# Performance work log

Measured on AMD Instinct MI355X. Metric: run time of the kernel, lower is better.

The kernel has to match this reference:

```python
import jax, jax.numpy as jnp
import numpy as np

EPS = 1e-6
ALPHA = 0.1
BETA = 0.25


def setup_inputs() -> dict:
    key = jax.random.key(0)
    k1, k2, k3 = jax.random.split(key, 3)
    B, C, D = 4096, 256, 128
    x = jax.random.normal(k1, (B, D), dtype=jnp.float32)
    prev_q = jax.random.normal(k2, (B, D), dtype=jnp.float32)
    codes = jax.random.normal(k3, (1, C, D), dtype=jnp.float32)
    return {"x": x, "prev_q": prev_q, "codes": codes}


def compute_distance(x, codes):
    # x: (B, D); codes: (1, C, D) or (B, 1, D) -> (B, C) / (B, 1); metric='l2'
    return jnp.sum((x[:, None, :] - codes) ** 2, axis=-1)


def get_rotation_matrix(u, v, eps=EPS):
    # u: (B, D) normalized; v: (D,) normalized -> R: (B, D, D)
    B, D = u.shape
    uvT = u[:, :, None] * v[None, None, :]          # (B, D, D) = u v^T
    vuT = v[None, :, None] * u[:, None, :]          # (B, D, D) = v u^T
    A = uvT - vuT
    A2 = jnp.einsum('bik,bkj->bij', A, A)
    dot = jnp.einsum('bd,d->b', u, v)[:, None, None]
    I = jnp.eye(D, dtype=u.dtype)
    return I + A + A2 / (1.0 + dot + eps)


def reference(x, prev_q, codes):
    B, D = x.shape
    v = jnp.ones((D,), dtype=x.dtype) / jnp.sqrt(jnp.asarray(D, x.dtype))
    # F.normalize(prev_q, dim=-1, eps=1e-6)
    n = jnp.linalg.norm(prev_q, axis=-1, keepdims=True)
    u = prev_q / jnp.maximum(n, EPS)
    R = get_rotation_matrix(u, v)
    # x_canonical = R^T x
    x_canonical = jnp.einsum('bji,bj->bi', R, x)
    raw_distances = compute_distance(x_canonical, codes)        # (B, C)
    distances = raw_distances / D / ALPHA
    # eval path: argmin + gather
    indices = jnp.argmin(distances, axis=-1)                    # (B,)
    quantized_canonical = codes[0][indices]                     # (B, D)
    quantized = jnp.einsum('bij,bj->bi', R, quantized_canonical)
    loss_commit = compute_distance(x, jax.lax.stop_gradient(quantized)[:, None, :]).mean()
    loss_codebook = compute_distance(jax.lax.stop_gradient(x), quantized[:, None, :]).mean()
    loss = loss_commit + BETA * loss_codebook
    return quantized, indices, loss
```

## Files before the change

kernel.cpp:

```cpp
#include <hip/hip_runtime.h>

#define BD 4096
#define CD 256
#define DD 128
#define RB 16
#define TB 1024

__global__ __launch_bounds__(TB) void rq_fused(
    const float* __restrict__ x,
    const float* __restrict__ pq,
    const float* __restrict__ codes,
    float* __restrict__ out)
{
    __shared__ __align__(16) char pool[CD * DD * 4
                                       + RB * DD * 4
                                       + CD * 4
                                       + RB * 4 * 4
                                       + RB * 4
                                       + RB * 4];
    float*  code_s = (float*)pool;
    float4* mb4    = (float4*)pool;
    float*  xc_s   = (float*)(pool + CD * DD * 4);
    float*  cn2_s  = xc_s + RB * DD;
    float*  row_c  = cn2_s + CD;
    float*  row_s  = row_c + RB;
    float*  row_invn = row_s + RB;
    int*    row_idx  = (int*)(row_invn + 2 * RB);
    float*  loss_s   = (float*)(row_idx + RB);

    const int tid  = threadIdx.x;
    const int wv   = tid >> 6;
    const int lane = tid & 63;
    const int row0 = blockIdx.x * RB;
    const float INV_SQRT_D = 0.088388347648318447f;

    const size_t growA = (size_t)(row0 + wv);
    const float2 xv = ((const float2*)(x  + growA * DD))[lane];
    const float2 pv = ((const float2*)(pq + growA * DD))[lane];

    {
        #pragma unroll
        for (int k = 0; k < 8; ++k) {
            const int f = k * TB + tid;
            const int g = f ^ ((f >> 5) & 7);
            __builtin_amdgcn_global_load_lds(
                (const __attribute__((address_space(1))) uint32_t*)(codes + (size_t)g * 4),
                (__attribute__((address_space(3))) uint32_t*)(code_s + (size_t)f * 4),
                16, 0, 0);
        }
    }

    {
        const int r = wv;
        float s0 = pv.x * pv.x + pv.y * pv.y;
        float s1 = pv.x + pv.y;
        float s2 = xv.x + xv.y;
        float s3 = pv.x * xv.x + pv.y * xv.y;
        #pragma unroll
        for (int m = 32; m > 0; m >>= 1) {
            s0 += __shfl_xor(s0, m);
            s1 += __shfl_xor(s1, m);
            s2 += __shfl_xor(s2, m);
            s3 += __shfl_xor(s3, m);
        }
        const float invn = 1.0f / fmaxf(sqrtf(s0), 1e-6f);
        const float b = s2 * INV_SQRT_D;
        const float a = s3 * invn;
        const float c = s1 * invn * INV_SQRT_D;
        const float s = 1.0f / (1.0f + c + 1e-6f);
        const float au = -b + s * (c * b - a);
        const float av =  a + s * (c * a - b);
        float2 o;
        o.x = xv.x + au * (pv.x * invn) + av * INV_SQRT_D;
        o.y = xv.y + au * (pv.y * invn) + av * INV_SQRT_D;
        ((float2*)(xc_s + r * DD))[lane] = o;
        if (lane == 0) { row_c[r] = c; row_s[r] = s; row_invn[r] = invn; }
    }
    __syncthreads();

    {
        const int c = tid >> 2, q = tid & 3;
        const int sw = c & 7;
        const float* cp = code_s + c * DD + q * 32;
        float n2 = 0.f;
        #pragma unroll
        for (int i = 0; i < 8; ++i) {
            const float4 v = *(const float4*)(cp + ((i ^ sw) << 2));
            n2 = fmaf(v.x, v.x, n2); n2 = fmaf(v.y, v.y, n2);
            n2 = fmaf(v.z, v.z, n2); n2 = fmaf(v.w, v.w, n2);
        }
        n2 += __shfl_xor(n2, 1);
        n2 += __shfl_xor(n2, 2);
        if (q == 0) cn2_s[c] = n2;
    }
    __syncthreads();

    const int rg = wv & 3, dq = wv >> 2;
    float xreg[4];
    #pragma unroll
    for (int rr = 0; rr < 4; ++rr)
        xreg[rr] = xc_s[(rg * 4 + rr) * DD + dq * 32 + (lane & 31)];
    const int sw = lane & 7;
    const float* cb = code_s + lane * DD + dq * 32;
    float acc[4][4] = {};
    #define RL(rr, j) __int_as_float(__builtin_amdgcn_readlane(__float_as_int(xreg[rr]), (j)))
    #pragma unroll
    for (int i = 0; i < 8; ++i) {
        const int off = (i ^ sw) << 2;
        const float4 c0 = *(const float4*)(cb + off);
        const float4 c1 = *(const float4*)(cb +  64 * DD + off);
        const float4 c2 = *(const float4*)(cb + 128 * DD + off);
        const float4 c3 = *(const float4*)(cb + 192 * DD + off);
        #pragma unroll
        for (int r = 0; r < 4; ++r) {
            const float y0 = RL(r, 4 * i + 0), y1 = RL(r, 4 * i + 1);
            const float y2 = RL(r, 4 * i + 2), y3 = RL(r, 4 * i + 3);
            acc[0][r] = fmaf(c0.x, y0, acc[0][r]); acc[0][r] = fmaf(c0.y, y1, acc[0][r]);
            acc[0][r] = fmaf(c0.z, y2, acc[0][r]); acc[0][r] = fmaf(c0.w, y3, acc[0][r]);
            acc[1][r] = fmaf(c1.x, y0, acc[1][r]); acc[1][r] = fmaf(c1.y, y1, acc[1][r]);
            acc[1][r] = fmaf(c1.z, y2, acc[1][r]); acc[1][r] = fmaf(c1.w, y3, acc[1][r]);
            acc[2][r] = fmaf(c2.x, y0, acc[2][r]); acc[2][r] = fmaf(c2.y, y1, acc[2][r]);
            acc[2][r] = fmaf(c2.z, y2, acc[2][r]); acc[2][r] = fmaf(c2.w, y3, acc[2][r]);
            acc[3][r] = fmaf(c3.x, y0, acc[3][r]); acc[3][r] = fmaf(c3.y, y1, acc[3][r]);
            acc[3][r] = fmaf(c3.z, y2, acc[3][r]); acc[3][r] = fmaf(c3.w, y3, acc[3][r]);
        }
    }
    #undef RL

    __syncthreads();
    if (dq != 0) {
        const int e = (rg * 3 + (dq - 1)) * 64 + lane;
        #pragma unroll
        for (int t = 0; t < 4; ++t) {
            float4 w;
            w.x = acc[t][0]; w.y = acc[t][1]; w.z = acc[t][2]; w.w = acc[t][3];
            mb4[t * 768 + e] = w;
        }
    }
    __syncthreads();
    if (dq == 0) {
        #pragma unroll
        for (int s = 0; s < 3; ++s) {
            const int e = (rg * 3 + s) * 64 + lane;
            #pragma unroll
            for (int t = 0; t < 4; ++t) {
                const float4 pm = mb4[t * 768 + e];
                acc[t][0] += pm.x; acc[t][1] += pm.y; acc[t][2] += pm.z; acc[t][3] += pm.w;
            }
        }
        const float cn0  = cn2_s[lane];
        const float cn1  = cn2_s[lane + 64];
        const float cn2v = cn2_s[lane + 128];
        const float cn3  = cn2_s[lane + 192];
        float bv[4]; int bi[4];
        #pragma unroll
        for (int r = 0; r < 4; ++r) {
            float v0 = fmaf(-2.f, acc[0][r], cn0); int i0 = lane;
            const float v1 = fmaf(-2.f, acc[1][r], cn1);
            const float v2 = fmaf(-2.f, acc[2][r], cn2v);
            const float v3 = fmaf(-2.f, acc[3][r], cn3);
            if (v1 < v0) { v0 = v1; i0 = lane + 64;  }
            if (v2 < v0) { v0 = v2; i0 = lane + 128; }
            if (v3 < v0) { v0 = v3; i0 = lane + 192; }
            bv[r] = v0; bi[r] = i0;
        }
        #pragma unroll
        for (int m = 1; m < 64; m <<= 1) {
            #pragma unroll
            for (int r = 0; r < 4; ++r) {
                const float ov = __shfl_xor(bv[r], m);
                const int   oi = __shfl_xor(bi[r], m);
                if (ov < bv[r] || (ov == bv[r] && oi < bi[r])) { bv[r] = ov; bi[r] = oi; }
            }
        }
        if (lane == 0) {
            #pragma unroll
            for (int r = 0; r < 4; ++r) {
                row_idx[rg * 4 + r] = bi[r];
                out[(size_t)BD * DD + row0 + rg * 4 + r] = (float)bi[r];
            }
        }
    }
    __syncthreads();

    {
        const int r = wv;
        const int qi = row_idx[r];
        const float invn = row_invn[r];
        const float c = row_c[r];
        const float s = row_s[r];
        const float2 q = ((const float2*)(codes + (size_t)qi * DD))[lane];
        float pd = pv.x * q.x + pv.y * q.y;
        float ws = q.x + q.y;
        #pragma unroll
        for (int m = 32; m > 0; m >>= 1) {
            pd += __shfl_xor(pd, m);
            ws += __shfl_xor(ws, m);
        }
        const float pp = pd * invn;
        const float w  = ws * INV_SQRT_D;
        const float bu  =  w + s * (c * w - pp);
        const float bvv = -pp + s * (c * pp - w);
        float2 o;
        o.x = q.x + bu * (pv.x * invn) + bvv * INV_SQRT_D;
        o.y = q.y + bu * (pv.y * invn) + bvv * INV_SQRT_D;
        ((float2*)(out + growA * DD))[lane] = o;

        float dx = xv.x - o.x;
        float ls = dx * dx;
        dx = xv.y - o.y;
        ls = fmaf(dx, dx, ls);
        #pragma unroll
        for (int m = 32; m > 0; m >>= 1) ls += __shfl_xor(ls, m);
        if (lane == 0) loss_s[r] = ls;
    }
    __syncthreads();
    if (tid == 0) {
        float tot = 0.f;
        #pragma unroll
        for (int r = 0; r < RB; ++r) tot += loss_s[r];
        atomicAdd(out + (size_t)BD * DD + BD, tot * (1.25f / (float)BD));
    }
}

extern "C" void kernel_launch(void* const* d_in, const int* in_sizes, int n_in,
                              void* d_out, int out_size, void* d_ws, size_t ws_size,
                              hipStream_t stream) {
    const float* xin   = (const float*)d_in[0];
    const float* prevq = (const float*)d_in[1];
    const float* codes = (const float*)d_in[2];
    float* out = (float*)d_out;
    rq_fused<<<BD / RB, TB, 0, stream>>>(xin, prevq, codes, out);
}
```

Measured before the change: 74.63 us.

## Halve rows per block and stage codebook in two halves to shrink LDS

Rows per block drop from 16 to 8 and the codebook is staged into LDS in two 128-code halves rather than all at once, halving the LDS footprint so more blocks can be resident per CU. Each half gets its own norm pass and distance pass. The async global_load_lds copy is replaced by register-staged float4 loads, and launch bounds now request higher occupancy. The trade-off is twice as many blocks, each re-reading the full codebook, plus extra barriers, and half of the waves sit idle during the per-row prologue and epilogue.

Result: slower. 78.52 us (+5.2%).

```diff
diff --git a/kernel.cpp b/kernel.cpp
--- a/kernel.cpp
+++ b/kernel.cpp
@@ -3,16 +3,17 @@
 #define BD 4096
 #define CD 256
 #define DD 128
-#define RB 16
+#define RB 8
 #define TB 1024
-
-__global__ __launch_bounds__(TB) void rq_fused(
+#define GRID (BD / RB)
+
+__global__ __launch_bounds__(TB, 8) void rq_fused(
     const float* __restrict__ x,
     const float* __restrict__ pq,
     const float* __restrict__ codes,
     float* __restrict__ out)
 {
-    __shared__ __align__(16) char pool[CD * DD * 4
+    __shared__ __align__(16) char pool[128 * DD * 4
                                        + RB * DD * 4
                                        + CD * 4
                                        + RB * 4 * 4
@@ -20,7 +21,7 @@
                                        + RB * 4];
     float*  code_s = (float*)pool;
     float4* mb4    = (float4*)pool;
-    float*  xc_s   = (float*)(pool + CD * DD * 4);
+    float*  xc_s   = (float*)(pool + 128 * DD * 4);
     float*  cn2_s  = xc_s + RB * DD;
     float*  row_c  = cn2_s + CD;
     float*  row_s  = row_c + RB;
@@ -34,23 +35,27 @@
     const int row0 = blockIdx.x * RB;
     const float INV_SQRT_D = 0.088388347648318447f;
 
-    const size_t growA = (size_t)(row0 + wv);
-    const float2 xv = ((const float2*)(x  + growA * DD))[lane];
-    const float2 pv = ((const float2*)(pq + growA * DD))[lane];
+    const size_t growA = (size_t)(row0 + (wv & 7));
+    float2 xv = {0.f, 0.f}, pv = {0.f, 0.f};
+    if (wv < 8) {
+        xv = ((const float2*)(x  + growA * DD))[lane];
+        pv = ((const float2*)(pq + growA * DD))[lane];
+    }
 
     {
-        #pragma unroll
-        for (int k = 0; k < 8; ++k) {
-            const int f = k * TB + tid;
-            const int g = f ^ ((f >> 5) & 7);
-            __builtin_amdgcn_global_load_lds(
-                (const __attribute__((address_space(1))) uint32_t*)(codes + (size_t)g * 4),
-                (__attribute__((address_space(3))) uint32_t*)(code_s + (size_t)f * 4),
-                16, 0, 0);
-        }
-    }
-
-    {
+        const float4* src = (const float4*)codes;
+        float4 t0, t1, t2, t3;
+        { int f = 0 * TB + tid; t0 = src[f ^ ((f >> 5) & 7)]; }
+        { int f = 1 * TB + tid; t1 = src[f ^ ((f >> 5) & 7)]; }
+        { int f = 2 * TB + tid; t2 = src[f ^ ((f >> 5) & 7)]; }
+        { int f = 3 * TB + tid; t3 = src[f ^ ((f >> 5) & 7)]; }
+        *(float4*)(code_s + (size_t)(0 * TB + tid) * 4) = t0;
+        *(float4*)(code_s + (size_t)(1 * TB + tid) * 4) = t1;
+        *(float4*)(code_s + (size_t)(2 * TB + tid) * 4) = t2;
+        *(float4*)(code_s + (size_t)(3 * TB + tid) * 4) = t3;
+    }
+
+    if (wv < 8) {
         const int r = wv;
         float s0 = pv.x * pv.x + pv.y * pv.y;
         float s1 = pv.x + pv.y;
@@ -78,87 +83,111 @@
     }
     __syncthreads();
 
+    const int rg = wv & 3, dq = wv >> 2;
+    const int sw = lane & 7;
+    const int c8  = tid >> 3;
+    const int oc8 = tid & 7;
+    const int sw8 = c8 & 7;
+    const float* cbB = code_s + lane * DD + dq * 32;
+    float accA[2][2], accB[2][2];
+
+    #define CN2_PASS(CH)                                                      \
+    {                                                                         \
+        const float* cp = code_s + c8 * DD;                                   \
+        float n2 = 0.f;                                                       \
+        _Pragma("unroll")                                                     \
+        for (int i = 0; i < 4; ++i) {                                         \
+            const int j = oc8 * 4 + i;                                        \
+            const float4 v = *(const float4*)(cp + ((j ^ sw8) << 2));         \
+            n2 = fmaf(v.x, v.x, n2); n2 = fmaf(v.y, v.y, n2);                 \
+            n2 = fmaf(v.z, v.z, n2); n2 = fmaf(v.w, v.w, n2);                 \
+        }                                                                     \
+        n2 += __shfl_xor(n2, 1);                                              \
+        n2 += __shfl_xor(n2, 2);                                              \
+        n2 += __shfl_xor(n2, 4);                                              \
+        if (oc8 == 0) cn2_s[(CH) * 128 + c8] = n2;                            \
+    }
+
+    #define RL(v, j) __int_as_float(__builtin_amdgcn_readlane(__float_as_int(v), (j)))
+    #define B_PASS(ACC)                                                       \
+    {                                                                         \
+        float xr0 = xc_s[(rg * 2 + 0) * DD + dq * 32 + (lane & 31)];          \
+        float xr1 = xc_s[(rg * 2 + 1) * DD + dq * 32 + (lane & 31)];          \
+        ACC[0][0] = 0.f; ACC[0][1] = 0.f; ACC[1][0] = 0.f; ACC[1][1] = 0.f;   \
+        _Pragma("unroll")                                                     \
+        for (int i = 0; i < 8; ++i) {                                         \
+            const int off = (i ^ sw) << 2;                                    \
+            const float4 c0 = *(const float4*)(cbB + off);                    \
+            const float4 c1 = *(const float4*)(cbB + 64 * DD + off);          \
+            const float y00 = RL(xr0, 4 * i + 0), y01 = RL(xr0, 4 * i + 1);   \
+            const float y02 = RL(xr0, 4 * i + 2), y03 = RL(xr0, 4 * i + 3);   \
+            const float y10 = RL(xr1, 4 * i + 0), y11 = RL(xr1, 4 * i + 1);   \
+            const float y12 = RL(xr1, 4 * i + 2), y13 = RL(xr1, 4 * i + 3);   \
+            ACC[0][0] = fmaf(c0.x, y00, ACC[0][0]); ACC[0][0] = fmaf(c0.y, y01, ACC[0][0]); \
+            ACC[0][0] = fmaf(c0.z, y02, ACC[0][0]); ACC[0][0] = fmaf(c0.w, y03, ACC[0][0]); \
+            ACC[0][1] = fmaf(c0.x, y10, ACC[0][1]); ACC[0][1] = fmaf(c0.y, y11, ACC[0][1]); \
+            ACC[0][1] = fmaf(c0.z, y12, ACC[0][1]); ACC[0][1] = fmaf(c0.w, y13, ACC[0][1]); \
+            ACC[1][0] = fmaf(c1.x, y00, ACC[1][0]); ACC[1][0] = fmaf(c1.y, y01, ACC[1][0]); \
+            ACC[1][0] = fmaf(c1.z, y02, ACC[1][0]); ACC[1][0] = fmaf(c1.w, y03, ACC[1][0]); \
+            ACC[1][1] = fmaf(c1.x, y10, ACC[1][1]); ACC[1][1] = fmaf(c1.y, y11, ACC[1][1]); \
+            ACC[1][1] = fmaf(c1.z, y12, ACC[1][1]); ACC[1][1] = fmaf(c1.w, y13, ACC[1][1]); \
+        }                                                                     \
+    }
+
+    CN2_PASS(0)
+    B_PASS(accA)
+    __syncthreads();
+
     {
-        const int c = tid >> 2, q = tid & 3;
-        const int sw = c & 7;
-        const float* cp = code_s + c * DD + q * 32;
-        float n2 = 0.f;
-        #pragma unroll
-        for (int i = 0; i < 8; ++i) {
-            const float4 v = *(const float4*)(cp + ((i ^ sw) << 2));
-            n2 = fmaf(v.x, v.x, n2); n2 = fmaf(v.y, v.y, n2);
-            n2 = fmaf(v.z, v.z, n2); n2 = fmaf(v.w, v.w, n2);
-        }
-        n2 += __shfl_xor(n2, 1);
-        n2 += __shfl_xor(n2, 2);
-        if (q == 0) cn2_s[c] = n2;
-    }
-    __syncthreads();
-
-    const int rg = wv & 3, dq = wv >> 2;
-    float xreg[4];
-    #pragma unroll
-    for (int rr = 0; rr < 4; ++rr)
-        xreg[rr] = xc_s[(rg * 4 + rr) * DD + dq * 32 + (lane & 31)];
-    const int sw = lane & 7;
-    const float* cb = code_s + lane * DD + dq * 32;
-    float acc[4][4] = {};
-    #define RL(rr, j) __int_as_float(__builtin_amdgcn_readlane(__float_as_int(xreg[rr]), (j)))
-    #pragma unroll
-    for (int i = 0; i < 8; ++i) {
-        const int off = (i ^ sw) << 2;
-        const float4 c0 = *(const float4*)(cb + off);
-        const float4 c1 = *(const float4*)(cb +  64 * DD + off);
-        const float4 c2 = *(const float4*)(cb + 128 * DD + off);
-        const float4 c3 = *(const float4*)(cb + 192 * DD + off);
-        #pragma unroll
-        for (int r = 0; r < 4; ++r) {
-            const float y0 = RL(r, 4 * i + 0), y1 = RL(r, 4 * i + 1);
-            const float y2 = RL(r, 4 * i + 2), y3 = RL(r, 4 * i + 3);
-            acc[0][r] = fmaf(c0.x, y0, acc[0][r]); acc[0][r] = fmaf(c0.y, y1, acc[0][r]);
-            acc[0][r] = fmaf(c0.z, y2, acc[0][r]); acc[0][r] = fmaf(c0.w, y3, acc[0][r]);
-            acc[1][r] = fmaf(c1.x, y0, acc[1][r]); acc[1][r] = fmaf(c1.y, y1, acc[1][r]);
-            acc[1][r] = fmaf(c1.z, y2, acc[1][r]); acc[1][r] = fmaf(c1.w, y3, acc[1][r]);
-            acc[2][r] = fmaf(c2.x, y0, acc[2][r]); acc[2][r] = fmaf(c2.y, y1, acc[2][r]);
-            acc[2][r] = fmaf(c2.z, y2, acc[2][r]); acc[2][r] = fmaf(c2.w, y3, acc[2][r]);
-            acc[3][r] = fmaf(c3.x, y0, acc[3][r]); acc[3][r] = fmaf(c3.y, y1, acc[3][r]);
-            acc[3][r] = fmaf(c3.z, y2, acc[3][r]); acc[3][r] = fmaf(c3.w, y3, acc[3][r]);
-        }
-    }
+        const float4* src = (const float4*)codes + 4096;
+        float4 t0, t1, t2, t3;
+        { int f = 0 * TB + tid; t0 = src[f ^ ((f >> 5) & 7)]; }
+        { int f = 1 * TB + tid; t1 = src[f ^ ((f >> 5) & 7)]; }
+        { int f = 2 * TB + tid; t2 = src[f ^ ((f >> 5) & 7)]; }
+        { int f = 3 * TB + tid; t3 = src[f ^ ((f >> 5) & 7)]; }
+        *(float4*)(code_s + (size_t)(0 * TB + tid) * 4) = t0;
+        *(float4*)(code_s + (size_t)(1 * TB + tid) * 4) = t1;
+        *(float4*)(code_s + (size_t)(2 * TB + tid) * 4) = t2;
+        *(float4*)(code_s + (size_t)(3 * TB + tid) * 4) = t3;
+    }
+    __syncthreads();
+
+    CN2_PASS(1)
+    B_PASS(accB)
+    __syncthreads();
     #undef RL
-
-    __syncthreads();
+    #undef B_PASS
+    #undef CN2_PASS
+
     if (dq != 0) {
         const int e = (rg * 3 + (dq - 1)) * 64 + lane;
-        #pragma unroll
-        for (int t = 0; t < 4; ++t) {
-            float4 w;
-            w.x = acc[t][0]; w.y = acc[t][1]; w.z = acc[t][2]; w.w = acc[t][3];
-            mb4[t * 768 + e] = w;
-        }
+        float4 w0, w1;
+        w0.x = accA[0][0]; w0.y = accA[0][1]; w0.z = accA[1][0]; w0.w = accA[1][1];
+        w1.x = accB[0][0]; w1.y = accB[0][1]; w1.z = accB[1][0]; w1.w = accB[1][1];
+        mb4[e]       = w0;
+        mb4[768 + e] = w1;
     }
     __syncthreads();
     if (dq == 0) {
         #pragma unroll
         for (int s = 0; s < 3; ++s) {
             const int e = (rg * 3 + s) * 64 + lane;
-            #pragma unroll
-            for (int t = 0; t < 4; ++t) {
-                const float4 pm = mb4[t * 768 + e];
-                acc[t][0] += pm.x; acc[t][1] += pm.y; acc[t][2] += pm.z; acc[t][3] += pm.w;
-            }
-        }
-        const float cn0  = cn2_s[lane];
-        const float cn1  = cn2_s[lane + 64];
+            const float4 p0 = mb4[e];
+            const float4 p1 = mb4[768 + e];
+            accA[0][0] += p0.x; accA[0][1] += p0.y; accA[1][0] += p0.z; accA[1][1] += p0.w;
+            accB[0][0] += p1.x; accB[0][1] += p1.y; accB[1][0] += p1.z; accB[1][1] += p1.w;
+        }
+        const float cn0 = cn2_s[lane];
+        const float cn1 = cn2_s[lane + 64];
         const float cn2v = cn2_s[lane + 128];
-        const float cn3  = cn2_s[lane + 192];
-        float bv[4]; int bi[4];
-        #pragma unroll
-        for (int r = 0; r < 4; ++r) {
-            float v0 = fmaf(-2.f, acc[0][r], cn0); int i0 = lane;
-            const float v1 = fmaf(-2.f, acc[1][r], cn1);
-            const float v2 = fmaf(-2.f, acc[2][r], cn2v);
-            const float v3 = fmaf(-2.f, acc[3][r], cn3);
+        const float cn3 = cn2_s[lane + 192];
+        float bv[2]; int bi[2];
+        #pragma unroll
+        for (int r = 0; r < 2; ++r) {
+            float v0 = fmaf(-2.f, accA[0][r], cn0); int i0 = lane;
+            const float v1 = fmaf(-2.f, accA[1][r], cn1);
+            const float v2 = fmaf(-2.f, accB[0][r], cn2v);
+            const float v3 = fmaf(-2.f, accB[1][r], cn3);
             if (v1 < v0) { v0 = v1; i0 = lane + 64;  }
             if (v2 < v0) { v0 = v2; i0 = lane + 128; }
             if (v3 < v0) { v0 = v3; i0 = lane + 192; }
@@ -167,7 +196,7 @@
         #pragma unroll
         for (int m = 1; m < 64; m <<= 1) {
             #pragma unroll
-            for (int r = 0; r < 4; ++r) {
+            for (int r = 0; r < 2; ++r) {
                 const float ov = __shfl_xor(bv[r], m);
                 const int   oi = __shfl_xor(bi[r], m);
                 if (ov < bv[r] || (ov == bv[r] && oi < bi[r])) { bv[r] = ov; bi[r] = oi; }
@@ -175,15 +204,15 @@
         }
         if (lane == 0) {
             #pragma unroll
-            for (int r = 0; r < 4; ++r) {
-                row_idx[rg * 4 + r] = bi[r];
-                out[(size_t)BD * DD + row0 + rg * 4 + r] = (float)bi[r];
+            for (int r = 0; r < 2; ++r) {
+                row_idx[rg * 2 + r] = bi[r];
+                out[(size_t)BD * DD + row0 + rg * 2 + r] = (float)bi[r];
             }
         }
     }
     __syncthreads();
 
-    {
+    if (wv < 8) {
         const int r = wv;
         const int qi = row_idx[r];
         const float invn = row_invn[r];
@@ -230,5 +259,5 @@
     const float* prevq = (const float*)d_in[1];
     const float* codes = (const float*)d_in[2];
     float* out = (float*)d_out;
-    rq_fused<<<BD / RB, TB, 0, stream>>>(xin, prevq, codes, out);
+    rq_fused<<<GRID, TB, 0, stream>>>(xin, prevq, codes, out);
 }
```
